# Optimization experiments

Measured on AMD Instinct MI355X. Metric: run time of the kernel, lower is better.

The kernel has to match this reference:

```python
import jax, jax.numpy as jnp
import numpy as np

B, TGT, SRC, DIM = 8, 1024, 1024, 1024

def setup_inputs() -> dict:
    key = jax.random.key(0)
    k1, k2, k3, k4, k5 = jax.random.split(key, 5)
    s = 1.0 / np.sqrt(DIM)
    return {
        "input": jax.random.normal(k1, (B, TGT, DIM), dtype=jnp.float32),
        "context": jax.random.normal(k2, (B, SRC, DIM), dtype=jnp.float32),
        "context_lengths": jax.random.randint(k3, (B,), 1, SRC + 1, dtype=jnp.int64 if jax.config.jax_enable_x64 else jnp.int32),
        "W_in": jax.random.normal(k4, (DIM, DIM), dtype=jnp.float32) * s,   # torch Linear weight [out,in]
        "W_out": jax.random.normal(k5, (DIM, 2 * DIM), dtype=jnp.float32) * s,
    }

def reference(input, context, context_lengths, W_in, W_out):
    # GlobalAttention, attn_type='general', include_rnn=True, dropout=0 (identity)
    # score: (W_in @ h_t) . h_s  -> [B, TGT, SRC]
    h_t = jnp.einsum('btd,ed->bte', input, W_in)
    align = jnp.einsum('bte,bse->bts', h_t, context)
    # mask positions >= length with -inf before softmax over source dim
    mask = jnp.arange(align.shape[-1])[None, :] < context_lengths[:, None]  # [B, SRC]
    align = jnp.where(mask[:, None, :], align, -jnp.inf)
    align_vectors = jax.nn.softmax(align, axis=-1)                         # [B, TGT, SRC]
    c = jnp.einsum('bts,bsd->btd', align_vectors, context)                 # context vector
    concat = jnp.concatenate([c, input], axis=-1)                          # [B, TGT, 2*DIM]
    attn_h = jnp.tanh(jnp.einsum('btf,df->btd', concat, W_out))            # linear_out (no bias) + tanh
    return attn_h, align_vectors
```

## Files before the change

### kernel.cpp

```cpp
#include <hip/hip_runtime.h>

typedef __attribute__((ext_vector_type(8))) short short8;
typedef __attribute__((ext_vector_type(4))) float f32x4;

#define DIM  1024
#define BT   8192
#define NBAT 8

__device__ __forceinline__ unsigned short f2bf(float x){
  union { float f; unsigned u; } un; un.f = x;
  unsigned r = un.u + 0x7fffu + ((un.u >> 16) & 1u);
  return (unsigned short)(r >> 16);
}
__device__ __forceinline__ float bf2f(unsigned short h){
  union { unsigned u; float f; } un; un.u = ((unsigned)h) << 16;
  return un.f;
}

__global__ void split_kernel(const float* __restrict__ x,
                             unsigned short* __restrict__ hi,
                             unsigned short* __restrict__ lo,
                             int n4){
  int stride = gridDim.x * blockDim.x;
  for (int i = blockIdx.x * blockDim.x + threadIdx.x; i < n4; i += stride){
    float4 v = ((const float4*)x)[i];
    ushort4 h, l;
    h.x = f2bf(v.x); l.x = f2bf(v.x - bf2f(h.x));
    h.y = f2bf(v.y); l.y = f2bf(v.y - bf2f(h.y));
    h.z = f2bf(v.z); l.z = f2bf(v.z - bf2f(h.z));
    h.w = f2bf(v.w); l.w = f2bf(v.w - bf2f(h.w));
    ((ushort4*)hi)[i] = h;
    ((ushort4*)lo)[i] = l;
  }
}

__global__ void transpose_kernel(const float* __restrict__ ctx,
                                 unsigned short* __restrict__ ctxT){
  __shared__ unsigned short t[64][65];
  int bz = blockIdx.z;
  int s0 = blockIdx.x << 6, d0 = blockIdx.y << 6;
  int tx = threadIdx.x, ty = threadIdx.y;
  const float* src = ctx + (((size_t)bz << 10) + s0) * DIM + d0;
  #pragma unroll
  for (int i = ty; i < 64; i += 4)
    t[i][tx] = f2bf(src[(size_t)i * DIM + tx]);
  __syncthreads();
  unsigned short* dst = ctxT + (((size_t)bz << 10) + d0) * DIM + s0;
  #pragma unroll
  for (int i = ty; i < 64; i += 4)
    dst[(size_t)i * DIM + tx] = t[tx][i];
}

__global__ __launch_bounds__(256) void softmax_kernel(float* __restrict__ sc,
                                                      unsigned short* __restrict__ Pb,
                                                      const int* __restrict__ lens){
  const int row = blockIdx.x;
  const int len = lens[row >> 10];
  const int tid = threadIdx.x;
  const int lane = tid & 63, wid = tid >> 6;
  float* rp = sc + ((size_t)row << 10);
  float4 v = ((const float4*)rp)[tid];
  const int s0 = tid << 2;
  float x0 = (s0 + 0 < len) ? v.x : -INFINITY;
  float x1 = (s0 + 1 < len) ? v.y : -INFINITY;
  float x2 = (s0 + 2 < len) ? v.z : -INFINITY;
  float x3 = (s0 + 3 < len) ? v.w : -INFINITY;
  float wmax = fmaxf(fmaxf(x0, x1), fmaxf(x2, x3));
  #pragma unroll
  for (int o = 32; o > 0; o >>= 1) wmax = fmaxf(wmax, __shfl_xor(wmax, o));
  __shared__ float red[8];
  if (lane == 0) red[wid] = wmax;
  __syncthreads();
  float mx = fmaxf(fmaxf(red[0], red[1]), fmaxf(red[2], red[3]));
  float e0 = (s0 + 0 < len) ? __expf(x0 - mx) : 0.f;
  float e1 = (s0 + 1 < len) ? __expf(x1 - mx) : 0.f;
  float e2 = (s0 + 2 < len) ? __expf(x2 - mx) : 0.f;
  float e3 = (s0 + 3 < len) ? __expf(x3 - mx) : 0.f;
  float ws = e0 + e1 + e2 + e3;
  #pragma unroll
  for (int o = 32; o > 0; o >>= 1) ws += __shfl_xor(ws, o);
  if (lane == 0) red[4 + wid] = ws;
  __syncthreads();
  float inv = 1.f / (red[4] + red[5] + red[6] + red[7]);
  float4 p; p.x = e0 * inv; p.y = e1 * inv; p.z = e2 * inv; p.w = e3 * inv;
  ((float4*)rp)[tid] = p;
  ushort4 pb; pb.x = f2bf(p.x); pb.y = f2bf(p.y); pb.z = f2bf(p.z); pb.w = f2bf(p.w);
  ((ushort4*)(Pb + ((size_t)row << 10)))[tid] = pb;
}

__device__ __forceinline__ int lds_off(int r, int kb){
  return r * 64 + (((kb ^ ((r >> 1) & 3))) << 4);
}

#define TILEA 16384
#define TILEB 8192

__device__ __forceinline__ void gld16(void* lds, const void* g){
  __builtin_amdgcn_global_load_lds(
      (__attribute__((address_space(1))) void*)(g),
      (__attribute__((address_space(3))) void*)(lds), 16, 0, 0);
}

template<int EPI, int NT, int KSPLIT, int SM>
__global__ __launch_bounds__(512, 2) void gemm_pipe_kernel(
    const unsigned short* __restrict__ Ah,  const unsigned short* __restrict__ Al,
    const unsigned short* __restrict__ Ah2, const unsigned short* __restrict__ Al2,
    const unsigned short* __restrict__ Bh,  const unsigned short* __restrict__ Bl,
    int lda, int ldb,
    float* __restrict__ outF, unsigned short* __restrict__ o1,
    unsigned short* __restrict__ o2, int ldo)
{
  constexpr int OFF_AL = TILEA;
  constexpr int OFF_BH = (SM == 0) ? 2 * TILEA : TILEA;
  constexpr int OFF_BL = OFF_BH + TILEB;
  constexpr int BUFSZ_T = OFF_BL + TILEB;

  __shared__ __align__(16) char sm0[BUFSZ_T];
  __shared__ __align__(16) char sm1[BUFSZ_T];
  __shared__ __align__(16) char sm2[BUFSZ_T];

  const int tid  = threadIdx.x;
  const int lane = tid & 63;
  const int w    = tid >> 6;

  int bx = blockIdx.x, by = blockIdx.y;
  {
    int o = bx + (by << 3);
    int xcd = o & 7, j = o >> 3;
    bx = j & 7;
    by = xcd * (gridDim.y >> 3) + (j >> 3);
  }
  const int m0 = by << 8;
  const int n0 = bx << 7;

  const unsigned short* gAh  = Ah  + (size_t)m0 * lda;
  const unsigned short* gAl  = Al  + (size_t)m0 * lda;
  const unsigned short* gAh2 = Ah2 + (size_t)m0 * lda;
  const unsigned short* gAl2 = Al2 + (size_t)m0 * lda;
  const unsigned short* gBh  = Bh  + (size_t)n0 * ldb;
  const unsigned short* gBl  = Bl  + (size_t)n0 * ldb;

  const int rA0 = (w << 5) + (lane >> 2);
  const int rA1 = rA0 + 16;
  const int rB0 = (w << 4) + (lane >> 2);
  const int cA0 = ((lane & 3) ^ ((rA0 >> 1) & 3)) << 3;
  const int cA1 = ((lane & 3) ^ ((rA1 >> 1) & 3)) << 3;
  const int cB0 = ((lane & 3) ^ ((rB0 >> 1) & 3)) << 3;
  const unsigned short* pAh0  = gAh  + (size_t)rA0 * lda + cA0;
  const unsigned short* pAh1  = gAh  + (size_t)rA1 * lda + cA1;
  const unsigned short* pAl0  = gAl  + (size_t)rA0 * lda + cA0;
  const unsigned short* pAl1  = gAl  + (size_t)rA1 * lda + cA1;
  const unsigned short* pAh20 = gAh2 + (size_t)rA0 * lda + cA0;
  const unsigned short* pAh21 = gAh2 + (size_t)rA1 * lda + cA1;
  const unsigned short* pAl20 = gAl2 + (size_t)rA0 * lda + cA0;
  const unsigned short* pAl21 = gAl2 + (size_t)rA1 * lda + cA1;
  const unsigned short* pBh0  = gBh  + (size_t)rB0 * ldb + cB0;
  const unsigned short* pBl0  = gBl  + (size_t)rB0 * ldb + cB0;
  const int dA0 = (w << 5) << 6;
  const int dA1 = dA0 + (16 << 6);
  const int dB0 = (w << 4) << 6;

  f32x4 acc[4][4];
  #pragma unroll
  for (int m = 0; m < 4; m++)
    #pragma unroll
    for (int n = 0; n < 4; n++)
      acc[m][n] = (f32x4){0.f, 0.f, 0.f, 0.f};

  const int wr = (w >> 1) << 6;
  const int wc = (w & 1) << 6;
  const int fr = lane & 15;
  const int kb = lane >> 4;

  short8 ah, al, bh[4], bl[4];

#define STAGE(WR, KS) do { int _k = (KS);                                   \
    const unsigned short *_s0, *_s1;                                        \
    if (KSPLIT < NT * 32 && _k >= KSPLIT){                                  \
      int _q = _k - KSPLIT;                                                 \
      _s0 = pAh20 + _q; _s1 = pAh21 + _q;                                   \
    } else { _s0 = pAh0 + _k; _s1 = pAh1 + _k; }                            \
    gld16(WR + dA0, _s0);                                                   \
    gld16(WR + dA1, _s1);                                                   \
    if constexpr (SM == 0){                                                 \
      const unsigned short *_s2, *_s3;                                      \
      if (KSPLIT < NT * 32 && _k >= KSPLIT){                                \
        int _q = _k - KSPLIT;                                               \
        _s2 = pAl20 + _q; _s3 = pAl21 + _q;                                 \
      } else { _s2 = pAl0 + _k; _s3 = pAl1 + _k; }                          \
      gld16(WR + OFF_AL + dA0, _s2);                                        \
      gld16(WR + OFF_AL + dA1, _s3);                                        \
    }                                                                       \
    gld16(WR + OFF_BH + dB0, pBh0 + _k);                                    \
    gld16(WR + OFF_BL + dB0, pBl0 + _k);                                    \
  } while(0)

#define READS_B(RD) do {                                                    \
    _Pragma("unroll")                                                       \
    for (int n = 0; n < 4; n++){                                            \
      int off = lds_off(wc + n * 16 + fr, kb);                              \
      bh[n] = *(const short8*)((RD) + OFF_BH + off);                        \
      bl[n] = *(const short8*)((RD) + OFF_BL + off);                        \
    }                                                                       \
  } while(0)

#define READS_A(RD, M) do {                                                 \
    int off = lds_off(wr + (M) * 16 + fr, kb);                              \
    ah = *(const short8*)((RD) + off);                                      \
    if constexpr (SM == 0) al = *(const short8*)((RD) + OFF_AL + off);      \
  } while(0)

#define MFMA_M(M) do {                                                      \
    __builtin_amdgcn_s_setprio(1);                                          \
    _Pragma("unroll")                                                       \
    for (int n = 0; n < 4; n++){                                            \
      acc[M][n] = __builtin_amdgcn_mfma_f32_16x16x32_bf16(ah, bh[n], acc[M][n], 0, 0, 0); \
      acc[M][n] = __builtin_amdgcn_mfma_f32_16x16x32_bf16(ah, bl[n], acc[M][n], 0, 0, 0); \
      if constexpr (SM == 0)                                                \
        acc[M][n] = __builtin_amdgcn_mfma_f32_16x16x32_bf16(al, bh[n], acc[M][n], 0, 0, 0); \
    }                                                                       \
    __builtin_amdgcn_s_setprio(0);                                          \
  } while(0)

#define BAR() do { __builtin_amdgcn_s_barrier();                            \
                   asm volatile("" ::: "memory"); } while(0)
#define LGKM0() asm volatile("s_waitcnt lgkmcnt(0)" ::: "memory")
#define VMCNT_STEP() do {                                                   \
    if constexpr (SM == 0) asm volatile("s_waitcnt vmcnt(6)" ::: "memory"); \
    else                   asm volatile("s_waitcnt vmcnt(4)" ::: "memory"); \
  } while(0)

#define STEP(RD, WR, T) do {                                                \
    int _ks = (((T) + 2 < NT) ? (T) + 2 : NT - 1) << 5;   \
    READS_B(RD); READS_A(RD, 0);                                            \
    STAGE(WR, _ks);                                                         \
    BAR(); LGKM0(); MFMA_M(0); BAR();                                       \
    READS_A(RD, 1);                                                        \
    BAR(); LGKM0(); MFMA_M(1); BAR();                                       \
    READS_A(RD, 2);                                                        \
    BAR(); LGKM0(); MFMA_M(2); BAR();                                       \
    READS_A(RD, 3);                                                        \
    BAR(); LGKM0(); MFMA_M(3);                                              \
    VMCNT_STEP();                                                           \
    BAR();                                                                  \
  } while(0)

  STAGE(sm0, 0);
  STAGE(sm1, 32);
  VMCNT_STEP();
  BAR();

  for (int t = 0; t < NT; t += 3){
    STEP(sm0, sm2, t);
    if (t + 1 < NT) STEP(sm1, sm0, t + 1);
    if (t + 2 < NT) STEP(sm2, sm1, t + 2);
  }
#undef STAGE
#undef READS_B
#undef READS_A
#undef MFMA_M
#undef BAR
#undef LGKM0
#undef VMCNT_STEP
#undef STEP

  const int rbase = (lane >> 4) << 2;
  const int cbase = lane & 15;
  #pragma unroll
  for (int m = 0; m < 4; m++){
    #pragma unroll
    for (int n = 0; n < 4; n++){
      f32x4 v = acc[m][n];
      int col = n0 + wc + n * 16 + cbase;
      #pragma unroll
      for (int j = 0; j < 4; j++){
        int row = m0 + wr + m * 16 + rbase + j;
        float val = v[j];
        size_t idx = (size_t)row * ldo + col;
        if (EPI == 0){
          unsigned short h = f2bf(val);
          o1[idx] = h;
          o2[idx] = f2bf(val - bf2f(h));
        } else {
          outF[idx] = tanhf(val);
        }
      }
    }
  }
}

template<bool SPLIT, int EPI>
__global__ __launch_bounds__(256, 2) void gemm_kernel(
    const unsigned short* __restrict__ Ah, const unsigned short* __restrict__ Al,
    const unsigned short* __restrict__ Bh, const unsigned short* __restrict__ Bl,
    int K, int lda, int ldb,
    long long aStride, long long bStride, long long oStride,
    float* __restrict__ outF, unsigned short* __restrict__ o1,
    unsigned short* __restrict__ o2, int ldo,
    const int* __restrict__ lens, int lmode)
{
  constexpr int TILE = 128 * 64;
  __shared__ char smem[(SPLIT ? 4 : 2) * TILE];
  char* sAh = smem;
  char* sBh = smem + TILE;
  char* sAl = smem + (SPLIT ? 2 : 0) * TILE;
  char* sBl = smem + (SPLIT ? 3 : 0) * TILE;

  const int tid  = threadIdx.x;
  const int lane = tid & 63;
  const int wid  = tid >> 6;
  const int z    = blockIdx.z;

  int bx = blockIdx.x, by = blockIdx.y;
  if (gridDim.x == 8 && gridDim.y == 8){
    int o = bx + (by << 3);
    int k = o & 7, j = o >> 3;
    bx = ((k & 3) << 1) | (j & 1);  by = ((k >> 2) << 2) | (j >> 1);
  }
  const int m0 = by * 128;
  const int n0 = bx * 128;

  int Keff = K;
  if (lmode){
    const int len = lens[z];
    if (lmode == 1 && n0 >= len) return;
    if (lmode == 2){
      int kc = (len + 31) & ~31;
      Keff = kc < K ? kc : K;
    }
  }

  const unsigned short* gAh = Ah + (size_t)z * aStride + (size_t)m0 * lda;
  const unsigned short* gBh = Bh + (size_t)z * bStride + (size_t)n0 * ldb;
  const unsigned short* gAl = SPLIT ? (Al + (size_t)z * aStride + (size_t)m0 * lda) : (const unsigned short*)0;
  const unsigned short* gBl = SPLIT ? (Bl + (size_t)z * bStride + (size_t)n0 * ldb) : (const unsigned short*)0;

  f32x4 acc[4][4];
  #pragma unroll
  for (int m = 0; m < 4; m++)
    #pragma unroll
    for (int n = 0; n < 4; n++)
      acc[m][n] = (f32x4){0.f, 0.f, 0.f, 0.f};

  const int wr = (wid >> 1) * 64;
  const int wc = (wid & 1) * 64;
  const int fr = lane & 15;
  const int kb = lane >> 4;

  for (int k0 = 0; k0 < Keff; k0 += 32){
    __syncthreads();
    #pragma unroll
    for (int it = 0; it < 2; ++it){
      int c = tid + it * 256;
      int r = c >> 2, kk = c & 3;
      int lo = lds_off(r, kk);
      size_t ga = (size_t)r * lda + k0 + kk * 8;
      size_t gb = (size_t)r * ldb + k0 + kk * 8;
      *(short8*)(sAh + lo) = *(const short8*)(gAh + ga);
      *(short8*)(sBh + lo) = *(const short8*)(gBh + gb);
      if (SPLIT){
        *(short8*)(sAl + lo) = *(const short8*)(gAl + ga);
        *(short8*)(sBl + lo) = *(const short8*)(gBl + gb);
      }
    }
    __syncthreads();

    short8 ah[4], bh[4], al[4], bl[4];
    #pragma unroll
    for (int m = 0; m < 4; m++){
      int off = lds_off(wr + m * 16 + fr, kb);
      ah[m] = *(const short8*)(sAh + off);
      if (SPLIT) al[m] = *(const short8*)(sAl + off);
    }
    #pragma unroll
    for (int n = 0; n < 4; n++){
      int off = lds_off(wc + n * 16 + fr, kb);
      bh[n] = *(const short8*)(sBh + off);
      if (SPLIT) bl[n] = *(const short8*)(sBl + off);
    }
    #pragma unroll
    for (int m = 0; m < 4; m++)
      #pragma unroll
      for (int n = 0; n < 4; n++){
        acc[m][n] = __builtin_amdgcn_mfma_f32_16x16x32_bf16(ah[m], bh[n], acc[m][n], 0, 0, 0);
        if (SPLIT){
          acc[m][n] = __builtin_amdgcn_mfma_f32_16x16x32_bf16(ah[m], bl[n], acc[m][n], 0, 0, 0);
          acc[m][n] = __builtin_amdgcn_mfma_f32_16x16x32_bf16(al[m], bh[n], acc[m][n], 0, 0, 0);
        }
      }
  }

  const int rbase = (lane >> 4) * 2 * 2;
  const int cbase = lane & 15;
  #pragma unroll
  for (int m = 0; m < 4; m++){
    #pragma unroll
    for (int n = 0; n < 4; n++){
      f32x4 v = acc[m][n];
      int col = n0 + wc + n * 16 + cbase;
      #pragma unroll
      for (int j = 0; j < 4; j++){
        int row = m0 + wr + m * 16 + rbase + j;
        float val = v[j];
        size_t idx = (size_t)row * ldo + col;
        if (EPI == 0){
          unsigned short h = f2bf(val);
          o1[(size_t)z * oStride + idx] = h;
          o2[(size_t)z * oStride + idx] = f2bf(val - bf2f(h));
        } else if (EPI == 1){
          outF[(size_t)z * oStride + idx] = val;
        } else if (EPI == 4){
          o1[(size_t)z * oStride + idx] = f2bf(val);
        } else {
          outF[idx] = tanhf(val);
        }
      }
    }
  }
}

extern "C" void kernel_launch(void* const* d_in, const int* in_sizes, int n_in,
                              void* d_out, int out_size, void* d_ws, size_t ws_size,
                              hipStream_t stream){
  const float* input   = (const float*)d_in[0];
  const float* context = (const float*)d_in[1];
  const int*   lens    = (const int*)d_in[2];
  const float* Win     = (const float*)d_in[3];
  const float* Wout    = (const float*)d_in[4];
  float* attn  = (float*)d_out;
  float* align = attn + (size_t)BT * DIM;

  char* ws = (char*)d_ws;
  size_t off = 0;
  auto alloc = [&](size_t bytes) -> char* {
    char* p = ws + off; off += (bytes + 255) & ~(size_t)255; return p;
  };
  const size_t MTD = (size_t)BT * DIM;
  unsigned short* in_hi = (unsigned short*)alloc(MTD * 2);
  unsigned short* in_lo = (unsigned short*)alloc(MTD * 2);
  unsigned short* cx_hi = (unsigned short*)alloc(MTD * 2);
  unsigned short* cx_lo = (unsigned short*)alloc(MTD * 2);
  unsigned short* wi_hi = (unsigned short*)alloc((size_t)DIM * DIM * 2);
  unsigned short* wi_lo = (unsigned short*)alloc((size_t)DIM * DIM * 2);
  unsigned short* ht_hi = (unsigned short*)alloc(MTD * 2);
  unsigned short* ht_lo = (unsigned short*)alloc(MTD * 2);
  unsigned short* cxT   = (unsigned short*)alloc(MTD * 2);
  unsigned short* c_hi  = (unsigned short*)alloc(MTD * 2);
  unsigned short* wo_hi = (unsigned short*)alloc((size_t)DIM * 2 * DIM * 2);
  unsigned short* wo_lo = (unsigned short*)alloc((size_t)DIM * 2 * DIM * 2);
  unsigned short* p_bf  = cx_hi;
  if (off > ws_size) return;

  split_kernel<<<4096, 256, 0, stream>>>(input, in_hi, in_lo, (int)(MTD >> 2));
  split_kernel<<<4096, 256, 0, stream>>>(context, cx_hi, cx_lo, (int)(MTD >> 2));
  split_kernel<<<1024, 256, 0, stream>>>(Win, wi_hi, wi_lo, (DIM * DIM) >> 2);
  split_kernel<<<2048, 256, 0, stream>>>(Wout, wo_hi, wo_lo, (DIM * 2 * DIM) >> 2);
  transpose_kernel<<<dim3(16, 16, NBAT), dim3(64, 4), 0, stream>>>(context, cxT);

  gemm_pipe_kernel<0, 32, 1024, 0><<<dim3(8, 32), 512, 0, stream>>>(
      in_hi, in_lo, in_hi, in_lo, wi_hi, wi_lo, DIM, DIM,
      nullptr, ht_hi, ht_lo, DIM);
  gemm_kernel<true, 1><<<dim3(8, 8, NBAT), 256, 0, stream>>>(
      ht_hi, ht_lo, cx_hi, cx_lo, DIM, DIM, DIM,
      (long long)DIM * 1024, (long long)DIM * 1024, (long long)DIM * 1024,
      align, nullptr, nullptr, DIM, lens, 1);
  softmax_kernel<<<BT, 256, 0, stream>>>(align, p_bf, lens);
  gemm_kernel<false, 4><<<dim3(8, 8, NBAT), 256, 0, stream>>>(
      p_bf, nullptr, cxT, nullptr, DIM, DIM, DIM,
      (long long)DIM * 1024, (long long)DIM * 1024, (long long)1024 * 1024,
      nullptr, c_hi, nullptr, DIM, lens, 2);
  gemm_pipe_kernel<3, 64, 1024, 1><<<dim3(8, 32), 512, 0, stream>>>(
      c_hi, c_hi, in_hi, in_hi, wo_hi, wo_lo, DIM, 2 * DIM,
      attn, nullptr, nullptr, DIM);
}
```

Measured before the change: 261.3 us.

## Fuse context split with transpose and add 4-wave GEMM for output projection

Merges the context hi/lo split into the transpose kernel so the fp32 context is read once instead of twice. Adds a new 256-thread GEMM kernel with 256x128 tiles, double buffering and two A fragments per MFMA group, and uses it for the final output projection. The older pipelined kernel loses its single-A-precision specialisation. The new kernel carries more accumulators per wave, which raises register pressure, and has fewer waves to hide latency.

After: 278.6 us. 6.6% more time.

```diff
diff --git a/kernel.cpp b/kernel.cpp
--- a/kernel.cpp
+++ b/kernel.cpp
@@ -34,16 +34,26 @@
   }
 }
 
-__global__ void transpose_kernel(const float* __restrict__ ctx,
-                                 unsigned short* __restrict__ ctxT){
+__global__ void ctx_prep_kernel(const float* __restrict__ ctx,
+                                unsigned short* __restrict__ hi,
+                                unsigned short* __restrict__ lo,
+                                unsigned short* __restrict__ ctxT){
   __shared__ unsigned short t[64][65];
   int bz = blockIdx.z;
   int s0 = blockIdx.x << 6, d0 = blockIdx.y << 6;
   int tx = threadIdx.x, ty = threadIdx.y;
-  const float* src = ctx + (((size_t)bz << 10) + s0) * DIM + d0;
-  #pragma unroll
-  for (int i = ty; i < 64; i += 4)
-    t[i][tx] = f2bf(src[(size_t)i * DIM + tx]);
+  const size_t base = (((size_t)bz << 10) + s0) * DIM + d0;
+  const float* src = ctx + base;
+  unsigned short* hrow = hi + base;
+  unsigned short* lrow = lo + base;
+  #pragma unroll
+  for (int i = ty; i < 64; i += 4){
+    float v = src[(size_t)i * DIM + tx];
+    unsigned short h = f2bf(v);
+    hrow[(size_t)i * DIM + tx] = h;
+    lrow[(size_t)i * DIM + tx] = f2bf(v - bf2f(h));
+    t[i][tx] = h;
+  }
   __syncthreads();
   unsigned short* dst = ctxT + (((size_t)bz << 10) + d0) * DIM + s0;
   #pragma unroll
@@ -92,16 +102,180 @@
   return r * 64 + (((kb ^ ((r >> 1) & 3))) << 4);
 }
 
-#define TILEA 16384
-#define TILEB 8192
-
 __device__ __forceinline__ void gld16(void* lds, const void* g){
   __builtin_amdgcn_global_load_lds(
       (__attribute__((address_space(1))) void*)(g),
       (__attribute__((address_space(3))) void*)(lds), 16, 0, 0);
 }
 
-template<int EPI, int NT, int KSPLIT, int SM>
+template<int EPI, int NT, int KSPLIT>
+__global__ __launch_bounds__(256, 2) void gemm_pipe4_kernel(
+    const unsigned short* __restrict__ Ah, const unsigned short* __restrict__ Ah2,
+    const unsigned short* __restrict__ Bh, const unsigned short* __restrict__ Bl,
+    int lda, int ldb,
+    float* __restrict__ outF, unsigned short* __restrict__ o1,
+    unsigned short* __restrict__ o2, int ldo)
+{
+  constexpr int OFF_BH = 16384;
+  constexpr int OFF_BL = OFF_BH + 8192;
+  constexpr int BUF = OFF_BL + 8192;
+
+  __shared__ __align__(16) char sm0[BUF];
+  __shared__ __align__(16) char sm1[BUF];
+
+  const int tid  = threadIdx.x;
+  const int lane = tid & 63;
+  const int w    = tid >> 6;
+
+  int bx = blockIdx.x, by = blockIdx.y;
+  {
+    int o = bx + (by << 3);
+    int xcd = o & 7, j = o >> 3;
+    bx = j & 7;
+    by = xcd * (gridDim.y >> 3) + (j >> 3);
+  }
+  const int m0 = by << 8;
+  const int n0 = bx << 7;
+
+  const unsigned short* gAh  = Ah  + (size_t)m0 * lda;
+  const unsigned short* gAh2 = Ah2 + (size_t)m0 * lda;
+  const unsigned short* gBh  = Bh  + (size_t)n0 * ldb;
+  const unsigned short* gBl  = Bl  + (size_t)n0 * ldb;
+
+  const unsigned short* pA[4];  const unsigned short* pA2[4]; int dA[4];
+  #pragma unroll
+  for (int i = 0; i < 4; i++){
+    int r = (w << 6) + (lane >> 2) + 16 * i;
+    int c = ((lane & 3) ^ ((r >> 1) & 3)) << 3;
+    pA[i]  = gAh  + (size_t)r * lda + c;
+    pA2[i] = gAh2 + (size_t)r * lda + c;
+    dA[i]  = ((w << 6) + 16 * i) << 6;
+  }
+  const unsigned short* pB[2];  const unsigned short* pBl2[2]; int dB[2];
+  #pragma unroll
+  for (int j = 0; j < 2; j++){
+    int r = (w << 5) + (lane >> 2) + 16 * j;
+    int c = ((lane & 3) ^ ((r >> 1) & 3)) << 3;
+    pB[j]   = gBh + (size_t)r * ldb + c;
+    pBl2[j] = gBl + (size_t)r * ldb + c;
+    dB[j]   = ((w << 5) + 16 * j) << 6;
+  }
+
+  f32x4 acc[8][4];
+  #pragma unroll
+  for (int m = 0; m < 8; m++)
+    #pragma unroll
+    for (int n = 0; n < 4; n++)
+      acc[m][n] = (f32x4){0.f, 0.f, 0.f, 0.f};
+
+  const int wr = (w >> 1) << 7;
+  const int wc = (w & 1) << 6;
+  const int fr = lane & 15;
+  const int kb = lane >> 4;
+
+  short8 a0, a1, bh[4], bl[4];
+
+#define STAGE4(WR, K0) do { int _k = (K0);                                  \
+    _Pragma("unroll")                                                       \
+    for (int i = 0; i < 4; i++){                                            \
+      const unsigned short* _s;                                             \
+      if (KSPLIT < NT * 32 && _k >= KSPLIT) _s = pA2[i] + (_k - KSPLIT);    \
+      else                                  _s = pA[i] + _k;                \
+      gld16(WR + dA[i], _s);                                                \
+    }                                                                       \
+    _Pragma("unroll")                                                       \
+    for (int j = 0; j < 2; j++){                                            \
+      gld16(WR + OFF_BH + dB[j], pB[j] + _k);                               \
+      gld16(WR + OFF_BL + dB[j], pBl2[j] + _k);                             \
+    }                                                                       \
+  } while(0)
+
+#define RB4(RD) do {                                                        \
+    _Pragma("unroll")                                                       \
+    for (int n = 0; n < 4; n++){                                            \
+      int off = lds_off(wc + n * 16 + fr, kb);                              \
+      bh[n] = *(const short8*)((RD) + OFF_BH + off);                        \
+      bl[n] = *(const short8*)((RD) + OFF_BL + off);                        \
+    }                                                                       \
+  } while(0)
+
+#define RA2(RD, M) do {                                                     \
+    a0 = *(const short8*)((RD) + lds_off(wr + (M) * 16 + fr, kb));          \
+    a1 = *(const short8*)((RD) + lds_off(wr + ((M)+1) * 16 + fr, kb));      \
+  } while(0)
+
+#define MM2(M) do {                                                         \
+    __builtin_amdgcn_s_setprio(1);                                          \
+    _Pragma("unroll")                                                       \
+    for (int n = 0; n < 4; n++){                                            \
+      acc[(M)][n]   = __builtin_amdgcn_mfma_f32_16x16x32_bf16(a0, bh[n], acc[(M)][n], 0, 0, 0);   \
+      acc[(M)][n]   = __builtin_amdgcn_mfma_f32_16x16x32_bf16(a0, bl[n], acc[(M)][n], 0, 0, 0);   \
+      acc[(M)+1][n] = __builtin_amdgcn_mfma_f32_16x16x32_bf16(a1, bh[n], acc[(M)+1][n], 0, 0, 0); \
+      acc[(M)+1][n] = __builtin_amdgcn_mfma_f32_16x16x32_bf16(a1, bl[n], acc[(M)+1][n], 0, 0, 0); \
+    }                                                                       \
+    __builtin_amdgcn_s_setprio(0);                                          \
+  } while(0)
+
+#define BAR() do { __builtin_amdgcn_s_barrier();                            \
+                   asm volatile("" ::: "memory"); } while(0)
+#define LGKM0() asm volatile("s_waitcnt lgkmcnt(0)" ::: "memory")
+
+#define STEP4(RD, WR, T) do {                                               \
+    RB4(RD); RA2(RD, 0);                                                    \
+    if ((T) + 1 < NT) STAGE4(WR, ((T) + 1) << 5);                           \
+    BAR(); LGKM0(); MM2(0); BAR();                                          \
+    RA2(RD, 2); BAR(); LGKM0(); MM2(2); BAR();                              \
+    RA2(RD, 4); BAR(); LGKM0(); MM2(4); BAR();                              \
+    RA2(RD, 6); BAR(); LGKM0(); MM2(6);                                     \
+    asm volatile("s_waitcnt vmcnt(0)" ::: "memory");                        \
+    BAR();                                                                  \
+  } while(0)
+
+  STAGE4(sm0, 0);
+  asm volatile("s_waitcnt vmcnt(0)" ::: "memory");
+  BAR();
+
+  for (int t = 0; t < NT; t += 2){
+    STEP4(sm0, sm1, t);
+    STEP4(sm1, sm0, t + 1);
+  }
+#undef STAGE4
+#undef RB4
+#undef RA2
+#undef MM2
+#undef BAR
+#undef LGKM0
+#undef STEP4
+
+  const int rbase = (lane >> 4) << 2;
+  const int cbase = lane & 15;
+  #pragma unroll
+  for (int m = 0; m < 8; m++){
+    #pragma unroll
+    for (int n = 0; n < 4; n++){
+      f32x4 v = acc[m][n];
+      int col = n0 + wc + n * 16 + cbase;
+      #pragma unroll
+      for (int j = 0; j < 4; j++){
+        int row = m0 + wr + m * 16 + rbase + j;
+        float val = v[j];
+        size_t idx = (size_t)row * ldo + col;
+        if (EPI == 0){
+          unsigned short h = f2bf(val);
+          o1[idx] = h;
+          o2[idx] = f2bf(val - bf2f(h));
+        } else {
+          outF[idx] = tanhf(val);
+        }
+      }
+    }
+  }
+}
+
+#define TILEA 16384
+#define TILEB 8192
+
+template<int EPI, int NT, int KSPLIT>
 __global__ __launch_bounds__(512, 2) void gemm_pipe_kernel(
     const unsigned short* __restrict__ Ah,  const unsigned short* __restrict__ Al,
     const unsigned short* __restrict__ Ah2, const unsigned short* __restrict__ Al2,
@@ -111,7 +285,7 @@
     unsigned short* __restrict__ o2, int ldo)
 {
   constexpr int OFF_AL = TILEA;
-  constexpr int OFF_BH = (SM == 0) ? 2 * TILEA : TILEA;
+  constexpr int OFF_BH = 2 * TILEA;
   constexpr int OFF_BL = OFF_BH + TILEB;
   constexpr int BUFSZ_T = OFF_BL + TILEB;
 
@@ -175,22 +349,15 @@
   short8 ah, al, bh[4], bl[4];
 
 #define STAGE(WR, KS) do { int _k = (KS);                                   \
-    const unsigned short *_s0, *_s1;                                        \
+    const unsigned short *_s0, *_s1, *_s2, *_s3;                            \
     if (KSPLIT < NT * 32 && _k >= KSPLIT){                                  \
       int _q = _k - KSPLIT;                                                 \
-      _s0 = pAh20 + _q; _s1 = pAh21 + _q;                                   \
-    } else { _s0 = pAh0 + _k; _s1 = pAh1 + _k; }                            \
+      _s0 = pAh20 + _q; _s1 = pAh21 + _q; _s2 = pAl20 + _q; _s3 = pAl21 + _q; \
+    } else { _s0 = pAh0 + _k; _s1 = pAh1 + _k; _s2 = pAl0 + _k; _s3 = pAl1 + _k; } \
     gld16(WR + dA0, _s0);                                                   \
     gld16(WR + dA1, _s1);                                                   \
-    if constexpr (SM == 0){                                                 \
-      const unsigned short *_s2, *_s3;                                      \
-      if (KSPLIT < NT * 32 && _k >= KSPLIT){                                \
-        int _q = _k - KSPLIT;                                               \
-        _s2 = pAl20 + _q; _s3 = pAl21 + _q;                                 \
-      } else { _s2 = pAl0 + _k; _s3 = pAl1 + _k; }                          \
-      gld16(WR + OFF_AL + dA0, _s2);                                        \
-      gld16(WR + OFF_AL + dA1, _s3);                                        \
-    }                                                                       \
+    gld16(WR + OFF_AL + dA0, _s2);                                          \
+    gld16(WR + OFF_AL + dA1, _s3);                                          \
     gld16(WR + OFF_BH + dB0, pBh0 + _k);                                    \
     gld16(WR + OFF_BL + dB0, pBl0 + _k);                                    \
   } while(0)
@@ -207,7 +374,7 @@
 #define READS_A(RD, M) do {                                                 \
     int off = lds_off(wr + (M) * 16 + fr, kb);                              \
     ah = *(const short8*)((RD) + off);                                      \
-    if constexpr (SM == 0) al = *(const short8*)((RD) + OFF_AL + off);      \
+    al = *(const short8*)((RD) + OFF_AL + off);                             \
   } while(0)
 
 #define MFMA_M(M) do {                                                      \
@@ -216,8 +383,7 @@
     for (int n = 0; n < 4; n++){                                            \
       acc[M][n] = __builtin_amdgcn_mfma_f32_16x16x32_bf16(ah, bh[n], acc[M][n], 0, 0, 0); \
       acc[M][n] = __builtin_amdgcn_mfma_f32_16x16x32_bf16(ah, bl[n], acc[M][n], 0, 0, 0); \
-      if constexpr (SM == 0)                                                \
-        acc[M][n] = __builtin_amdgcn_mfma_f32_16x16x32_bf16(al, bh[n], acc[M][n], 0, 0, 0); \
+      acc[M][n] = __builtin_amdgcn_mfma_f32_16x16x32_bf16(al, bh[n], acc[M][n], 0, 0, 0); \
     }                                                                       \
     __builtin_amdgcn_s_setprio(0);                                          \
   } while(0)
@@ -225,10 +391,6 @@
 #define BAR() do { __builtin_amdgcn_s_barrier();                            \
                    asm volatile("" ::: "memory"); } while(0)
 #define LGKM0() asm volatile("s_waitcnt lgkmcnt(0)" ::: "memory")
-#define VMCNT_STEP() do {                                                   \
-    if constexpr (SM == 0) asm volatile("s_waitcnt vmcnt(6)" ::: "memory"); \
-    else                   asm volatile("s_waitcnt vmcnt(4)" ::: "memory"); \
-  } while(0)
 
 #define STEP(RD, WR, T) do {                                                \
     int _ks = (((T) + 2 < NT) ? (T) + 2 : NT - 1) << 5;   \
@@ -241,13 +403,13 @@
     BAR(); LGKM0(); MFMA_M(2); BAR();                                       \
     READS_A(RD, 3);                                                        \
     BAR(); LGKM0(); MFMA_M(3);                                              \
-    VMCNT_STEP();                                                           \
+    asm volatile("s_waitcnt vmcnt(6)" ::: "memory");                        \
     BAR();                                                                  \
   } while(0)
 
   STAGE(sm0, 0);
   STAGE(sm1, 32);
-  VMCNT_STEP();
+  asm volatile("s_waitcnt vmcnt(6)" ::: "memory");
   BAR();
 
   for (int t = 0; t < NT; t += 3){
@@ -261,7 +423,6 @@
 #undef MFMA_M
 #undef BAR
 #undef LGKM0
-#undef VMCNT_STEP
 #undef STEP
 
   const int rbase = (lane >> 4) << 2;
@@ -452,12 +613,11 @@
   if (off > ws_size) return;
 
   split_kernel<<<4096, 256, 0, stream>>>(input, in_hi, in_lo, (int)(MTD >> 2));
-  split_kernel<<<4096, 256, 0, stream>>>(context, cx_hi, cx_lo, (int)(MTD >> 2));
   split_kernel<<<1024, 256, 0, stream>>>(Win, wi_hi, wi_lo, (DIM * DIM) >> 2);
   split_kernel<<<2048, 256, 0, stream>>>(Wout, wo_hi, wo_lo, (DIM * 2 * DIM) >> 2);
-  transpose_kernel<<<dim3(16, 16, NBAT), dim3(64, 4), 0, stream>>>(context, cxT);
-
-  gemm_pipe_kernel<0, 32, 1024, 0><<<dim3(8, 32), 512, 0, stream>>>(
+  ctx_prep_kernel<<<dim3(16, 16, NBAT), dim3(64, 4), 0, stream>>>(context, cx_hi, cx_lo, cxT);
+
+  gemm_pipe_kernel<0, 32, 1024><<<dim3(8, 32), 512, 0, stream>>>(
       in_hi, in_lo, in_hi, in_lo, wi_hi, wi_lo, DIM, DIM,
       nullptr, ht_hi, ht_lo, DIM);
   gemm_kernel<true, 1><<<dim3(8, 8, NBAT), 256, 0, stream>>>(
@@ -469,7 +629,7 @@
       p_bf, nullptr, cxT, nullptr, DIM, DIM, DIM,
       (long long)DIM * 1024, (long long)DIM * 1024, (long long)1024 * 1024,
       nullptr, c_hi, nullptr, DIM, lens, 2);
-  gemm_pipe_kernel<3, 64, 1024, 1><<<dim3(8, 32), 512, 0, stream>>>(
-      c_hi, c_hi, in_hi, in_hi, wo_hi, wo_lo, DIM, 2 * DIM,
+  gemm_pipe4_kernel<3, 64, 1024><<<dim3(8, 32), 256, 0, stream>>>(
+      c_hi, in_hi, wo_hi, wo_lo, DIM, 2 * DIM,
       attn, nullptr, nullptr, DIM);
 }
```
